# Optimization experiments

Measured on AMD Instinct MI355X. Metric: run time of the kernel, lower is better.

Reference implementation:

```python
import jax, jax.numpy as jnp
import numpy as np
import math

B, T, C, F = 8, 2048, 1024, 4096
N_LAYER, LAYER_ID = 12, 1


def _init_params(key):
    ks = jax.random.split(key, 16)
    s = 0.02
    ratio_0_to_1 = LAYER_ID / (N_LAYER - 1)
    ratio_1_to_almost0 = 1.0 - LAYER_ID / N_LAYER
    h = np.arange(C, dtype=np.float32)
    decay = -5.0 + 8.0 * (h / (C - 1)) ** (0.7 + 1.3 * ratio_0_to_1)
    zigzag = np.array([((i + 1) % 3 - 1) for i in range(C)], dtype=np.float32) * 0.5
    first = np.ones(C, dtype=np.float32) * math.log(0.3) + zigzag
    xi = (np.arange(C, dtype=np.float32) / C)
    p = {
        'ln1_w': jnp.ones(C), 'ln1_b': jnp.zeros(C),
        'ln2_w': jnp.ones(C), 'ln2_b': jnp.zeros(C),
        'att_time_decay': jnp.asarray(decay),
        'att_time_first': jnp.asarray(first),
        'att_mix_k': jnp.asarray(xi ** ratio_1_to_almost0),
        'att_mix_v': jnp.asarray(xi ** ratio_1_to_almost0 + 0.3 * ratio_0_to_1),
        'att_mix_r': jnp.asarray(xi ** (0.5 * ratio_1_to_almost0)),
        'att_Wk': jax.random.normal(ks[0], (C, C)) * s,
        'att_Wv': jax.random.normal(ks[1], (C, C)) * s,
        'att_Wr': jax.random.normal(ks[2], (C, C)) * s,
        'att_Wo': jax.random.normal(ks[3], (C, C)) * s,
        'ffn_mix_k': jnp.asarray(xi ** ratio_1_to_almost0),
        'ffn_mix_r': jnp.asarray(xi ** ratio_1_to_almost0),
        'ffn_Wk': jax.random.normal(ks[4], (F, C)) * s,
        'ffn_Wr': jax.random.normal(ks[5], (C, C)) * s,
        'ffn_Wv': jax.random.normal(ks[6], (C, F)) * s,
        'short_W': jax.random.normal(ks[7], (C, C)) * s,
    }
    return p


def setup_inputs() -> dict:
    key = jax.random.key(0)
    k1, k2 = jax.random.split(key)
    inp = {'x': jax.random.normal(k1, (B, T, C), dtype=jnp.float32)}
    inp.update(_init_params(k2))
    return inp


def _layernorm(x, w, b, eps=1e-5):
    mu = jnp.mean(x, axis=-1, keepdims=True)
    var = jnp.var(x, axis=-1, keepdims=True)
    return (x - mu) * jax.lax.rsqrt(var + eps) * w + b


def _time_shift(x):
    # ZeroPad2d((0,0,1,-1)): prepend zero row along T, drop last
    return jnp.pad(x, ((0, 0), (1, 0), (0, 0)))[:, :-1]


def _wkv(time_decay, time_first, k, v):
    # numerically-stable WKV recurrence, matching the CUDA kernel math
    w = -jnp.exp(time_decay)  # [C]
    u = time_first            # [C]
    kt = jnp.swapaxes(k, 0, 1)  # [T,B,C]
    vt = jnp.swapaxes(v, 0, 1)
    a0 = jnp.zeros(k.shape[::2] if False else (k.shape[0], k.shape[2]), k.dtype)
    b0 = jnp.zeros_like(a0)
    p0 = jnp.full_like(a0, -1e30)

    def step(carry, kv):
        a, b, p = carry
        k_t, v_t = kv
        ww = u + k_t
        q = jnp.maximum(p, ww)
        e1 = jnp.exp(p - q)
        e2 = jnp.exp(ww - q)
        y = (e1 * a + e2 * v_t) / (e1 * b + e2)
        ww2 = p + w
        q2 = jnp.maximum(ww2, k_t)
        f1 = jnp.exp(ww2 - q2)
        f2 = jnp.exp(k_t - q2)
        return (f1 * a + f2 * v_t, f1 * b + f2, q2), y

    _, ys = jax.lax.scan(step, (a0, b0, p0), (kt, vt))
    return jnp.swapaxes(ys, 0, 1)  # [B,T,C]


def _lin(x, W):
    return jnp.einsum('btc,oc->bto', x, W)


def reference(x, ln1_w, ln1_b, ln2_w, ln2_b,
              att_time_decay, att_time_first, att_mix_k, att_mix_v, att_mix_r,
              att_Wk, att_Wv, att_Wr, att_Wo,
              ffn_mix_k, ffn_mix_r, ffn_Wk, ffn_Wr, ffn_Wv, short_W):
    # --- TimeMix on ln1(x) ---
    h = _layernorm(x, ln1_w, ln1_b)
    hh = _time_shift(h)
    xk = h * att_mix_k + hh * (1 - att_mix_k)
    xv = h * att_mix_v + hh * (1 - att_mix_v)
    xr = h * att_mix_r + hh * (1 - att_mix_r)
    k = _lin(xk, att_Wk)
    v = _lin(xv, att_Wv)
    sr = jax.nn.sigmoid(_lin(xr, att_Wr))
    rwkv = sr * _wkv(att_time_decay, att_time_first, k, v)
    att_out = _lin(rwkv, att_Wo)
    # shortcut linear replaces identity residual (L3TC Block)
    x = _lin(x, short_W) + att_out
    # --- ChannelMix on ln2(x) ---
    g = _layernorm(x, ln2_w, ln2_b)
    gg = _time_shift(g)
    gk = g * ffn_mix_k + gg * (1 - ffn_mix_k)
    gr = g * ffn_mix_r + gg * (1 - ffn_mix_r)
    kk = jnp.square(jax.nn.relu(_lin(gk, ffn_Wk)))
    kv = _lin(kk, ffn_Wv)
    rkv = jax.nn.sigmoid(_lin(gr, ffn_Wr)) * kv
    return x + rkv
```

## Files before the change

### kernel.cpp

```cpp
#include <hip/hip_runtime.h>

#define BB 8
#define TT 2048
#define CC 1024
#define FF 4096
#define MM (BB*TT)

typedef unsigned short u16;
typedef __bf16 bf16x8 __attribute__((ext_vector_type(8)));
typedef float f32x4 __attribute__((ext_vector_type(4)));

__device__ __forceinline__ u16 f2bf(float f) {
  unsigned int u = __float_as_uint(f);
  u += 0x7fffu + ((u >> 16) & 1u);
  return (u16)(u >> 16);
}
__device__ __forceinline__ float bf2f(u16 h) {
  unsigned int u = ((unsigned int)h) << 16;
  return __uint_as_float(u);
}
__device__ __forceinline__ float sigm(float x) { return 1.f / (1.f + __expf(-x)); }

__device__ __forceinline__ void async16(const void* g, void* l) {
  __builtin_amdgcn_global_load_lds(
      (const __attribute__((address_space(1))) unsigned int*)g,
      (__attribute__((address_space(3))) unsigned int*)l, 16, 0, 0);
}

#define GROUP_M 16

template<int MODE>
__device__ __forceinline__ void gemm_body(
    const u16* __restrict__ A, const u16* __restrict__ W,
    float* __restrict__ Cf, u16* __restrict__ Cb,
    const u16* __restrict__ R, int N, int K)
{
  __shared__ __align__(16) u16 ldsA[128 * 32];
  __shared__ __align__(16) u16 ldsB[128 * 32];
  const int tid  = threadIdx.x;
  const int wave = tid >> 6;
  const int lane = tid & 63;

  const int bid  = blockIdx.x + blockIdx.y * gridDim.x;
  const int gsz  = GROUP_M * gridDim.y;
  const int gid  = bid / gsz;
  const int rem  = bid - gid * gsz;
  const int bm   = (gid * GROUP_M + (rem % GROUP_M)) * 128;
  const int bn   = (rem / GROUP_M) * 128;

  const int wm = (wave >> 1) * 64;
  const int wn = (wave & 1) * 64;
  const int lm = lane & 15;
  const int lq = lane >> 4;

  const int r_in = lane >> 2;
  const int cp   = lane & 3;
  const int cg   = cp ^ ((r_in >> 1) & 3);
  const int rA0  = wave * 16 + r_in;
  const int rA1  = 64 + rA0;
  const u16* gA0 = A + (size_t)(bm + rA0) * K + cg * 8;
  const u16* gA1 = A + (size_t)(bm + rA1) * K + cg * 8;
  const u16* gB0 = W + (size_t)(bn + rA0) * K + cg * 8;
  const u16* gB1 = W + (size_t)(bn + rA1) * K + cg * 8;
  u16* lA0 = &ldsA[(wave * 16) * 32];
  u16* lA1 = &ldsA[(64 + wave * 16) * 32];
  u16* lB0 = &ldsB[(wave * 16) * 32];
  u16* lB1 = &ldsB[(64 + wave * 16) * 32];

  const int crd  = lq ^ ((lm >> 1) & 3);
  const int offA0 = (wm + lm) * 32 + crd * 8;
  const int offB0 = (wn + lm) * 32 + crd * 8;

  f32x4 acc[4][4] = {};

  for (int kt = 0; kt < K; kt += 32) {
    async16(gA0 + kt, lA0);
    async16(gA1 + kt, lA1);
    async16(gB0 + kt, lB0);
    async16(gB1 + kt, lB1);
    __syncthreads();
    bf16x8 bfr[4];
#pragma unroll
    for (int ni = 0; ni < 4; ++ni)
      bfr[ni] = *(const bf16x8*)&ldsB[offB0 + ni * 16 * 32];
#pragma unroll
    for (int mi = 0; mi < 4; ++mi) {
      bf16x8 afr = *(const bf16x8*)&ldsA[offA0 + mi * 16 * 32];
#pragma unroll
      for (int ni = 0; ni < 4; ++ni)
        acc[mi][ni] = __builtin_amdgcn_mfma_f32_16x16x32_bf16(afr, bfr[ni], acc[mi][ni], 0, 0, 0);
    }
    __syncthreads();
  }

  const int row0 = bm + wm + lq * 4;
  const int col0 = bn + wn + lm;
#pragma unroll
  for (int mi = 0; mi < 4; ++mi)
#pragma unroll
    for (int ni = 0; ni < 4; ++ni) {
      size_t base = (size_t)(row0 + mi * 16) * N + (col0 + ni * 16);
#pragma unroll
      for (int r2 = 0; r2 < 4; ++r2) {
        size_t idx = base + (size_t)r2 * N;
        float v = acc[mi][ni][r2];
        if (MODE == 0) Cf[idx] = v;
        if (MODE == 2) { float rl = v > 0.f ? v : 0.f; Cb[idx] = f2bf(rl * rl); }
        if (MODE == 3) Cb[idx] = f2bf(v);
        if (MODE == 4) Cf[idx] += sigm(bf2f(R[idx])) * v;
      }
    }
}

template<int MODE>
__global__ __launch_bounds__(256, 2) void gemm_bt(
    const u16* __restrict__ A, const u16* __restrict__ W,
    float* __restrict__ Cf, u16* __restrict__ Cb,
    const u16* __restrict__ R, int N, int K)
{
  gemm_body<MODE>(A, W, Cf, Cb, R, N, K);
}

__global__ __launch_bounds__(256) void prep_mix(
    const float* __restrict__ x,
    const float* __restrict__ lnw, const float* __restrict__ lnb,
    const float* __restrict__ mk, const float* __restrict__ mv, const float* __restrict__ mr,
    u16* __restrict__ ok, u16* __restrict__ ov, u16* __restrict__ orr,
    u16* __restrict__ oxb)
{
  const int m = blockIdx.x;
  const int t = m & (TT - 1);
  const int tid = threadIdx.x;
  const int wave = tid >> 6, lane = tid & 63;
  const bool hasp = (t != 0);

  const float4 xc4 = ((const float4*)(x + (size_t)m * CC))[tid];
  float4 xp4 = make_float4(0.f, 0.f, 0.f, 0.f);
  if (hasp) xp4 = ((const float4*)(x + (size_t)(m - 1) * CC))[tid];

  float s0 = xc4.x + xc4.y + xc4.z + xc4.w;
  float s1 = xc4.x*xc4.x + xc4.y*xc4.y + xc4.z*xc4.z + xc4.w*xc4.w;
  float s2 = xp4.x + xp4.y + xp4.z + xp4.w;
  float s3 = xp4.x*xp4.x + xp4.y*xp4.y + xp4.z*xp4.z + xp4.w*xp4.w;
#pragma unroll
  for (int off2 = 32; off2 > 0; off2 >>= 1) {
    s0 += __shfl_xor(s0, off2);
    s1 += __shfl_xor(s1, off2);
    s2 += __shfl_xor(s2, off2);
    s3 += __shfl_xor(s3, off2);
  }
  __shared__ float red[4][4];
  if (lane == 0) { red[0][wave] = s0; red[1][wave] = s1; red[2][wave] = s2; red[3][wave] = s3; }
  __syncthreads();
  const float S0 = red[0][0] + red[0][1] + red[0][2] + red[0][3];
  const float S1 = red[1][0] + red[1][1] + red[1][2] + red[1][3];
  const float S2 = red[2][0] + red[2][1] + red[2][2] + red[2][3];
  const float S3 = red[3][0] + red[3][1] + red[3][2] + red[3][3];
  const float inv = 1.f / (float)CC;
  const float muc = S0 * inv, varc = S1 * inv - muc * muc, rsc = rsqrtf(varc + 1e-5f);
  const float mup = S2 * inv, varp = S3 * inv - mup * mup, rsp = rsqrtf(varp + 1e-5f);

  const float xc[4] = {xc4.x, xc4.y, xc4.z, xc4.w};
  const float xp[4] = {xp4.x, xp4.y, xp4.z, xp4.w};
  const float4 lw4 = ((const float4*)lnw)[tid];
  const float4 lb4 = ((const float4*)lnb)[tid];
  const float lw[4] = {lw4.x, lw4.y, lw4.z, lw4.w};
  const float lb[4] = {lb4.x, lb4.y, lb4.z, lb4.w};
  const float4 mk4 = ((const float4*)mk)[tid];
  const float mka[4] = {mk4.x, mk4.y, mk4.z, mk4.w};
  const float4 mr4 = ((const float4*)mr)[tid];
  const float mra[4] = {mr4.x, mr4.y, mr4.z, mr4.w};
  float mva[4] = {0.f, 0.f, 0.f, 0.f};
  if (ov) {
    const float4 mv4 = ((const float4*)mv)[tid];
    mva[0] = mv4.x; mva[1] = mv4.y; mva[2] = mv4.z; mva[3] = mv4.w;
  }

  ushort4 wk2, wv2, wr2, wb2;
  u16* pk = (u16*)&wk2; u16* pv = (u16*)&wv2; u16* pr = (u16*)&wr2; u16* pb = (u16*)&wb2;
#pragma unroll
  for (int j = 0; j < 4; ++j) {
    float h  = (xc[j] - muc) * rsc * lw[j] + lb[j];
    float hh = hasp ? (xp[j] - mup) * rsp * lw[j] + lb[j] : 0.f;
    pk[j] = f2bf(h * mka[j] + hh * (1.f - mka[j]));
    pv[j] = f2bf(h * mva[j] + hh * (1.f - mva[j]));
    pr[j] = f2bf(h * mra[j] + hh * (1.f - mra[j]));
    pb[j] = f2bf(xc[j]);
  }
  ((ushort4*)(ok + (size_t)m * CC))[tid] = wk2;
  if (ov)  ((ushort4*)(ov  + (size_t)m * CC))[tid] = wv2;
  ((ushort4*)(orr + (size_t)m * CC))[tid] = wr2;
  if (oxb) ((ushort4*)(oxb + (size_t)m * (2 * CC)))[tid] = wb2;
}

#define WKV_CPB 32
#define WKV_NCH 32
#define WKV_L   (TT / WKV_NCH)

__global__ __launch_bounds__(1024) void wkv_scan(
    const u16* __restrict__ k, const u16* __restrict__ v, const u16* __restrict__ r,
    const float* __restrict__ decay, const float* __restrict__ first,
    u16* __restrict__ out)
{
  const int b  = blockIdx.x >> 5;
  const int c0 = (blockIdx.x & 31) * WKV_CPB;
  const int tid = threadIdx.x;
  const int cl = tid & 31;
  const int j  = tid >> 5;
  const int c  = c0 + cl;

  const float w   = -__expf(decay[c]);
  const float lam = __expf(w);
  const float eu  = __expf(first[c]);

  const size_t base  = (size_t)b * TT * CC + (size_t)j * WKV_L * CC + c;
  size_t obase = ((size_t)b * TT + (size_t)j * WKV_L) * (2 * CC) + c;

  float a = 0.f, bb = 0.f;
  size_t idx = base;
  for (int i = 0; i < WKV_L; ++i, idx += CC) {
    const float kt = bf2f(k[idx]), vt = bf2f(v[idx]);
    const float ek = __expf(kt);
    a  = fmaf(lam, a, ek * vt);
    bb = fmaf(lam, bb, ek);
  }

  __shared__ float sA[WKV_NCH][WKV_CPB];
  __shared__ float sB[WKV_NCH][WKV_CPB];
  sA[j][cl] = a; sB[j][cl] = bb;
  __syncthreads();
  if (tid < WKV_CPB) {
    float ca = 0.f, cb = 0.f;
    const float cw   = -__expf(decay[c0 + tid]);
    const float cLam = __expf(cw * (float)WKV_L);
#pragma unroll
    for (int q = 0; q < WKV_NCH; ++q) {
      const float ta = sA[q][tid], tb = sB[q][tid];
      sA[q][tid] = ca; sB[q][tid] = cb;
      ca = fmaf(cLam, ca, ta);
      cb = fmaf(cLam, cb, tb);
    }
  }
  __syncthreads();
  a = sA[j][cl]; bb = sB[j][cl];

  idx = base;
  for (int i = 0; i < WKV_L; ++i, idx += CC, obase += 2 * CC) {
    const float kt = bf2f(k[idx]), vt = bf2f(v[idx]), rt = bf2f(r[idx]);
    const float ek = __expf(kt);
    const float e2 = eu * ek;
    const float y  = (a + e2 * vt) / (bb + e2);
    out[obase] = f2bf(sigm(rt) * y);
    a  = fmaf(lam, a, ek * vt);
    bb = fmaf(lam, bb, ek);
  }
}

struct ConvArgs { const float* src[8]; int end[8]; int dstoff[8]; };

__global__ __launch_bounds__(256) void conv_w(ConvArgs args, u16* __restrict__ dst)
{
  const int i = (blockIdx.x * 256 + threadIdx.x) * 4;
  int seg = 0;
  const float* sp = args.src[0];
  int base = 0;
#pragma unroll
  for (int s = 1; s < 8; ++s) {
    if (i >= args.end[s - 1]) { seg = s; sp = args.src[s]; base = args.end[s - 1]; }
  }
  const int l = i - base;
  const float4 vv = *(const float4*)(sp + l);
  int dsti;
  if (seg == 3)      { int row = l >> 10, col = l & 1023; dsti = args.dstoff[3] + row * 2048 + 1024 + col; }
  else if (seg == 4) { int row = l >> 10, col = l & 1023; dsti = args.dstoff[4] + row * 2048 + col; }
  else               dsti = args.dstoff[seg] + l;
  ushort4 d;
  d.x = f2bf(vv.x); d.y = f2bf(vv.y); d.z = f2bf(vv.z); d.w = f2bf(vv.w);
  *(ushort4*)(dst + dsti) = d;
}

extern "C" void kernel_launch(void* const* d_in, const int* in_sizes, int n_in,
                              void* d_out, int out_size, void* d_ws, size_t ws_size,
                              hipStream_t stream)
{
  const float* x    = (const float*)d_in[0];
  const float* ln1w = (const float*)d_in[1];
  const float* ln1b = (const float*)d_in[2];
  const float* ln2w = (const float*)d_in[3];
  const float* ln2b = (const float*)d_in[4];
  const float* tdec = (const float*)d_in[5];
  const float* tfir = (const float*)d_in[6];
  const float* amk  = (const float*)d_in[7];
  const float* amv  = (const float*)d_in[8];
  const float* amr  = (const float*)d_in[9];
  const float* Wk   = (const float*)d_in[10];
  const float* Wv   = (const float*)d_in[11];
  const float* Wr   = (const float*)d_in[12];
  const float* Wo   = (const float*)d_in[13];
  const float* fmk  = (const float*)d_in[14];
  const float* fmr  = (const float*)d_in[15];
  const float* WfK  = (const float*)d_in[16];
  const float* WfR  = (const float*)d_in[17];
  const float* WfV  = (const float*)d_in[18];
  const float* Wsh  = (const float*)d_in[19];
  float* out = (float*)d_out;
  char* ws = (char*)d_ws;

  u16* wW = (u16*)(ws);
  u16* U0 = (u16*)(ws + 29360128);
  u16* U1 = (u16*)(ws + 62914560);
  u16* U2 = (u16*)(ws + 96468992);
  u16* U3 = (u16*)(ws + 130023424);
  u16* U4 = (u16*)(ws + 163577856);

  u16* xk   = U0;
  u16* xv   = U1;
  u16* xr   = U2;
  u16* Ap   = U4;
  u16* kbuf = U3;
  u16* vbuf = U0;
  u16* rbuf = U1;
  u16* gk   = U0;
  u16* gr   = U1;
  u16* kkb  = U2;
  u16* rffn = U0;

  u16* bWk   = wW + 0;
  u16* bWv   = wW + 1048576;
  u16* bWr   = wW + 2097152;
  u16* bWsWo = wW + 3145728;
  u16* bWfR  = wW + 5242880;
  u16* bWfK  = wW + 6291456;
  u16* bWfV  = wW + 10485760;

  ConvArgs ca;
  ca.src[0] = Wk;  ca.src[1] = Wv;  ca.src[2] = Wr;  ca.src[3] = Wo;
  ca.src[4] = Wsh; ca.src[5] = WfR; ca.src[6] = WfK; ca.src[7] = WfV;
  const int e = 1048576;
  ca.end[0] = e;     ca.end[1] = 2*e;  ca.end[2] = 3*e;  ca.end[3] = 4*e;
  ca.end[4] = 5*e;   ca.end[5] = 6*e;  ca.end[6] = 10*e; ca.end[7] = 14*e;
  ca.dstoff[0] = 0;     ca.dstoff[1] = e;    ca.dstoff[2] = 2*e;
  ca.dstoff[3] = 3*e;   ca.dstoff[4] = 3*e;
  ca.dstoff[5] = 5*e;   ca.dstoff[6] = 6*e;  ca.dstoff[7] = 10*e;

  conv_w<<<14336, 256, 0, stream>>>(ca, wW);
  prep_mix<<<MM, 256, 0, stream>>>(x, ln1w, ln1b, amk, amv, amr, xk, xv, xr, Ap);

  dim3 g8(MM / 128, CC / 128);
  gemm_bt<3><<<g8, 256, 0, stream>>>(xk, bWk, nullptr, kbuf, nullptr, CC, CC);
  gemm_bt<3><<<g8, 256, 0, stream>>>(xv, bWv, nullptr, vbuf, nullptr, CC, CC);
  gemm_bt<3><<<g8, 256, 0, stream>>>(xr, bWr, nullptr, rbuf, nullptr, CC, CC);

  wkv_scan<<<BB * (CC / WKV_CPB), 1024, 0, stream>>>(kbuf, vbuf, rbuf, tdec, tfir, Ap + CC);

  gemm_bt<0><<<g8, 256, 0, stream>>>(Ap, bWsWo, out, nullptr, nullptr, CC, 2 * CC);

  prep_mix<<<MM, 256, 0, stream>>>(out, ln2w, ln2b, fmk, nullptr, fmr, gk, nullptr, gr, nullptr);

  dim3 gF(MM / 128, FF / 128);
  gemm_bt<2><<<gF, 256, 0, stream>>>(gk, bWfK, nullptr, kkb, nullptr, FF, CC);
  gemm_bt<3><<<g8, 256, 0, stream>>>(gr, bWfR, nullptr, rffn, nullptr, CC, CC);
  gemm_bt<4><<<g8, 256, 0, stream>>>(kkb, bWfV, out, nullptr, rffn, CC, FF);
}
```

Measured before the change: 904.1 us.

## Rewrite GEMM as 256x256 tile, 8-wave, double-buffered pipelined MFMA kernel

Replaces the 128x128, 4-wave, single-buffer GEMM with a 256x256 tile computed by 8 waves. LDS is double-buffered with BK=64 and XOR swizzling, and async global-to-LDS loads for the next tiles are interleaved with four MFMA phases. Explicit barriers, s_setprio and sched_barrier control the overlap. The aim is to hide load latency and raise arithmetic intensity. In exchange it uses much more LDS and registers, and the grid becomes coarse (256 blocks for the N=1024 GEMMs), which may leave the 256 CUs poorly balanced.

After: 836.5 us. 1.08x faster.

```diff
diff --git a/kernel.cpp b/kernel.cpp
--- a/kernel.cpp
+++ b/kernel.cpp
@@ -29,74 +29,170 @@
 
 #define GROUP_M 16
 
+#define DSR(d, a) asm volatile("ds_read_b128 %0, %1" : "=v"(d) : "v"(a))
+#define MFMA16(A_, B_, C_) \
+  (C_) = __builtin_amdgcn_mfma_f32_16x16x32_bf16( \
+      __builtin_bit_cast(bf16x8, (A_)), __builtin_bit_cast(bf16x8, (B_)), (C_), 0, 0, 0)
+
+#define PH_MID() do { \
+  __builtin_amdgcn_s_barrier(); \
+  asm volatile("s_waitcnt lgkmcnt(0)"); \
+  __builtin_amdgcn_sched_barrier(0); \
+  __builtin_amdgcn_s_setprio(1); } while (0)
+
+#define PH_END() do { \
+  __builtin_amdgcn_s_setprio(0); \
+  __builtin_amdgcn_sched_barrier(0); \
+  __builtin_amdgcn_s_barrier(); } while (0)
+
 template<int MODE>
-__device__ __forceinline__ void gemm_body(
+__global__ __launch_bounds__(512, 2) void gemm_bt(
     const u16* __restrict__ A, const u16* __restrict__ W,
     float* __restrict__ Cf, u16* __restrict__ Cb,
     const u16* __restrict__ R, int N, int K)
 {
-  __shared__ __align__(16) u16 ldsA[128 * 32];
-  __shared__ __align__(16) u16 ldsB[128 * 32];
+  __shared__ __align__(16) u16 ldsA[2][256 * 64];
+  __shared__ __align__(16) u16 ldsB[2][256 * 64];
+
   const int tid  = threadIdx.x;
   const int wave = tid >> 6;
   const int lane = tid & 63;
+  const int wmi  = wave >> 2;
+  const int wni  = wave & 3;
+  const int lm   = lane & 15;
+  const int lq   = lane >> 4;
 
   const int bid  = blockIdx.x + blockIdx.y * gridDim.x;
   const int gsz  = GROUP_M * gridDim.y;
   const int gid  = bid / gsz;
   const int rem  = bid - gid * gsz;
-  const int bm   = (gid * GROUP_M + (rem % GROUP_M)) * 128;
-  const int bn   = (rem / GROUP_M) * 128;
-
-  const int wm = (wave >> 1) * 64;
-  const int wn = (wave & 1) * 64;
-  const int lm = lane & 15;
-  const int lq = lane >> 4;
-
-  const int r_in = lane >> 2;
-  const int cp   = lane & 3;
-  const int cg   = cp ^ ((r_in >> 1) & 3);
-  const int rA0  = wave * 16 + r_in;
-  const int rA1  = 64 + rA0;
-  const u16* gA0 = A + (size_t)(bm + rA0) * K + cg * 8;
-  const u16* gA1 = A + (size_t)(bm + rA1) * K + cg * 8;
-  const u16* gB0 = W + (size_t)(bn + rA0) * K + cg * 8;
-  const u16* gB1 = W + (size_t)(bn + rA1) * K + cg * 8;
-  u16* lA0 = &ldsA[(wave * 16) * 32];
-  u16* lA1 = &ldsA[(64 + wave * 16) * 32];
-  u16* lB0 = &ldsB[(wave * 16) * 32];
-  u16* lB1 = &ldsB[(64 + wave * 16) * 32];
-
-  const int crd  = lq ^ ((lm >> 1) & 3);
-  const int offA0 = (wm + lm) * 32 + crd * 8;
-  const int offB0 = (wn + lm) * 32 + crd * 8;
-
-  f32x4 acc[4][4] = {};
-
-  for (int kt = 0; kt < K; kt += 32) {
-    async16(gA0 + kt, lA0);
-    async16(gA1 + kt, lA1);
-    async16(gB0 + kt, lB0);
-    async16(gB1 + kt, lB1);
-    __syncthreads();
-    bf16x8 bfr[4];
-#pragma unroll
-    for (int ni = 0; ni < 4; ++ni)
-      bfr[ni] = *(const bf16x8*)&ldsB[offB0 + ni * 16 * 32];
+  const int bm   = (gid * GROUP_M + (rem % GROUP_M)) * 256;
+  const int bn   = (rem / GROUP_M) * 256;
+
+  const int NT = K >> 6;
+
+  const int srow   = wave * 8 + (lane >> 3);
+  const int schunk = (lane & 7) ^ (lane >> 3);
+  const u16* gA = A + (size_t)(bm + srow) * K + schunk * 8;
+  const u16* gB = W + (size_t)(bn + srow) * K + schunk * 8;
+  const size_t rowK = (size_t)64 * K;
+
+  auto stA = [&](int buf, int q, int t2) {
+    async16(gA + (size_t)t2 * 64 + (size_t)q * rowK,
+            &ldsA[buf][(q * 64 + wave * 8) * 64]);
+  };
+  auto stB = [&](int buf, int q, int t2) {
+    async16(gB + (size_t)t2 * 64 + (size_t)q * rowK,
+            &ldsB[buf][(q * 64 + wave * 8) * 64]);
+  };
+
+  const unsigned lAbase =
+      (unsigned)(size_t)(const __attribute__((address_space(3))) u16*)&ldsA[0][0];
+  const unsigned lBbase =
+      (unsigned)(size_t)(const __attribute__((address_space(3))) u16*)&ldsB[0][0];
+  const unsigned aof0 = (unsigned)((wmi * 128 + lm) * 128 + (((lq    ) ^ (lm & 7)) * 16));
+  const unsigned aof1 = (unsigned)((wmi * 128 + lm) * 128 + (((lq + 4) ^ (lm & 7)) * 16));
+  const unsigned bof0 = (unsigned)((wni *  64 + lm) * 128 + (((lq    ) ^ (lm & 7)) * 16));
+  const unsigned bof1 = (unsigned)((wni *  64 + lm) * 128 + (((lq + 4) ^ (lm & 7)) * 16));
+
+  f32x4 acc[8][4] = {};
+  f32x4 a0[4][2], a1[4][2], b[2][2];
+
+  stA(0, 0, 0); stA(0, 1, 0); stA(0, 2, 0); stA(0, 3, 0);
+  stB(0, 0, 0); stB(0, 1, 0); stB(0, 2, 0); stB(0, 3, 0);
+  stA(1, 0, 1); stA(1, 2, 1); stA(1, 1, 1); stA(1, 3, 1);
+  stB(1, 0, 1); stB(1, 1, 1);
+  asm volatile("s_waitcnt vmcnt(4)");
+  __builtin_amdgcn_s_barrier();
+#pragma unroll
+  for (int mi = 0; mi < 4; ++mi) {
+    DSR(a0[mi][0], lAbase + aof0 + mi * 2048);
+    DSR(a0[mi][1], lAbase + aof1 + mi * 2048);
+  }
+
+  for (int t = 0; t < NT; ++t) {
+    const int cur = t & 1, nxt = cur ^ 1;
+    const unsigned cA = lAbase + cur * 32768;
+    const unsigned cB = lBbase + cur * 32768;
+    const unsigned nA = lAbase + nxt * 32768;
+    const bool s2 = (t + 2 < NT);
+    const bool s1 = (t + 1 < NT);
+
+#pragma unroll
+    for (int ni = 0; ni < 2; ++ni) {
+      DSR(b[ni][0], cB + bof0 + ni * 2048);
+      DSR(b[ni][1], cB + bof1 + ni * 2048);
+    }
+    if (s2) { stA(cur, 0, t + 2); stA(cur, 2, t + 2); }
+    if (s1) { stB(nxt, 2, t + 1); stB(nxt, 3, t + 1); }
+    PH_MID();
+#pragma unroll
+    for (int mi = 0; mi < 4; ++mi)
+#pragma unroll
+      for (int ni = 0; ni < 2; ++ni) {
+        MFMA16(a0[mi][0], b[ni][0], acc[mi][ni]);
+        MFMA16(a0[mi][1], b[ni][1], acc[mi][ni]);
+      }
+    PH_END();
+
 #pragma unroll
     for (int mi = 0; mi < 4; ++mi) {
-      bf16x8 afr = *(const bf16x8*)&ldsA[offA0 + mi * 16 * 32];
-#pragma unroll
-      for (int ni = 0; ni < 4; ++ni)
-        acc[mi][ni] = __builtin_amdgcn_mfma_f32_16x16x32_bf16(afr, bfr[ni], acc[mi][ni], 0, 0, 0);
-    }
-    __syncthreads();
-  }
-
-  const int row0 = bm + wm + lq * 4;
-  const int col0 = bn + wn + lm;
-#pragma unroll
-  for (int mi = 0; mi < 4; ++mi)
+      DSR(a1[mi][0], cA + aof0 + (4 + mi) * 2048);
+      DSR(a1[mi][1], cA + aof1 + (4 + mi) * 2048);
+    }
+    PH_MID();
+#pragma unroll
+    for (int mi = 0; mi < 4; ++mi)
+#pragma unroll
+      for (int ni = 0; ni < 2; ++ni) {
+        MFMA16(a1[mi][0], b[ni][0], acc[4 + mi][ni]);
+        MFMA16(a1[mi][1], b[ni][1], acc[4 + mi][ni]);
+      }
+    PH_END();
+
+#pragma unroll
+    for (int ni = 0; ni < 2; ++ni) {
+      DSR(b[ni][0], cB + bof0 + (2 + ni) * 2048);
+      DSR(b[ni][1], cB + bof1 + (2 + ni) * 2048);
+    }
+    if (s2) { stA(cur, 1, t + 2); stA(cur, 3, t + 2); }
+    PH_MID();
+#pragma unroll
+    for (int mi = 0; mi < 4; ++mi)
+#pragma unroll
+      for (int ni = 0; ni < 2; ++ni) {
+        MFMA16(a0[mi][0], b[ni][0], acc[mi][2 + ni]);
+        MFMA16(a0[mi][1], b[ni][1], acc[mi][2 + ni]);
+      }
+    PH_END();
+
+    if (s1) {
+#pragma unroll
+      for (int mi = 0; mi < 4; ++mi) {
+        DSR(a0[mi][0], nA + aof0 + mi * 2048);
+        DSR(a0[mi][1], nA + aof1 + mi * 2048);
+      }
+    }
+    if (s2) { stB(cur, 0, t + 2); stB(cur, 1, t + 2); }
+    PH_MID();
+#pragma unroll
+    for (int mi = 0; mi < 4; ++mi)
+#pragma unroll
+      for (int ni = 0; ni < 2; ++ni) {
+        MFMA16(a1[mi][0], b[ni][0], acc[4 + mi][2 + ni]);
+        MFMA16(a1[mi][1], b[ni][1], acc[4 + mi][2 + ni]);
+      }
+    __builtin_amdgcn_s_setprio(0);
+    __builtin_amdgcn_sched_barrier(0);
+    if (t < NT - 2) asm volatile("s_waitcnt vmcnt(4)");
+    else            asm volatile("s_waitcnt vmcnt(0)");
+    __builtin_amdgcn_s_barrier();
+  }
+
+  const int row0 = bm + wmi * 128 + lq * 4;
+  const int col0 = bn + wni * 64 + lm;
+#pragma unroll
+  for (int mi = 0; mi < 8; ++mi)
 #pragma unroll
     for (int ni = 0; ni < 4; ++ni) {
       size_t base = (size_t)(row0 + mi * 16) * N + (col0 + ni * 16);
@@ -110,15 +206,6 @@
         if (MODE == 4) Cf[idx] += sigm(bf2f(R[idx])) * v;
       }
     }
-}
-
-template<int MODE>
-__global__ __launch_bounds__(256, 2) void gemm_bt(
-    const u16* __restrict__ A, const u16* __restrict__ W,
-    float* __restrict__ Cf, u16* __restrict__ Cb,
-    const u16* __restrict__ R, int N, int K)
-{
-  gemm_body<MODE>(A, W, Cf, Cb, R, N, K);
 }
 
 __global__ __launch_bounds__(256) void prep_mix(
@@ -346,19 +433,19 @@
   conv_w<<<14336, 256, 0, stream>>>(ca, wW);
   prep_mix<<<MM, 256, 0, stream>>>(x, ln1w, ln1b, amk, amv, amr, xk, xv, xr, Ap);
 
-  dim3 g8(MM / 128, CC / 128);
-  gemm_bt<3><<<g8, 256, 0, stream>>>(xk, bWk, nullptr, kbuf, nullptr, CC, CC);
-  gemm_bt<3><<<g8, 256, 0, stream>>>(xv, bWv, nullptr, vbuf, nullptr, CC, CC);
-  gemm_bt<3><<<g8, 256, 0, stream>>>(xr, bWr, nullptr, rbuf, nullptr, CC, CC);
+  dim3 g8(MM / 256, CC / 256);
+  gemm_bt<3><<<g8, 512, 0, stream>>>(xk, bWk, nullptr, kbuf, nullptr, CC, CC);
+  gemm_bt<3><<<g8, 512, 0, stream>>>(xv, bWv, nullptr, vbuf, nullptr, CC, CC);
+  gemm_bt<3><<<g8, 512, 0, stream>>>(xr, bWr, nullptr, rbuf, nullptr, CC, CC);
 
   wkv_scan<<<BB * (CC / WKV_CPB), 1024, 0, stream>>>(kbuf, vbuf, rbuf, tdec, tfir, Ap + CC);
 
-  gemm_bt<0><<<g8, 256, 0, stream>>>(Ap, bWsWo, out, nullptr, nullptr, CC, 2 * CC);
+  gemm_bt<0><<<g8, 512, 0, stream>>>(Ap, bWsWo, out, nullptr, nullptr, CC, 2 * CC);
 
   prep_mix<<<MM, 256, 0, stream>>>(out, ln2w, ln2b, fmk, nullptr, fmr, gk, nullptr, gr, nullptr);
 
-  dim3 gF(MM / 128, FF / 128);
-  gemm_bt<2><<<gF, 256, 0, stream>>>(gk, bWfK, nullptr, kkb, nullptr, FF, CC);
-  gemm_bt<3><<<g8, 256, 0, stream>>>(gr, bWfR, nullptr, rffn, nullptr, CC, CC);
-  gemm_bt<4><<<g8, 256, 0, stream>>>(kkb, bWfV, out, nullptr, rffn, CC, FF);
-}
+  dim3 gF(MM / 256, FF / 256);
+  gemm_bt<2><<<gF, 512, 0, stream>>>(gk, bWfK, nullptr, kkb, nullptr, FF, CC);
+  gemm_bt<3><<<g8, 512, 0, stream>>>(gr, bWfR, nullptr, rffn, nullptr, CC, CC);
+  gemm_bt<4><<<g8, 512, 0, stream>>>(kkb, bWfV, out, nullptr, rffn, CC, FF);
+}
```
